# Kernel tuning notes

Measured on AMD Instinct MI355X. Metric: run time of the kernel, lower is better.

Reference implementation:

```python
import jax, jax.numpy as jnp
import numpy as np

N_NODES = 20000
N_EDGES = 320000
F_IN = 256      # num_features_mol
HIDDEN = 512    # hidden_size


def _glorot(key, shape):
    fan_in, fan_out = shape
    lim = jnp.sqrt(6.0 / (fan_in + fan_out)).astype(jnp.float32)
    return jax.random.uniform(key, shape, jnp.float32, -lim, lim)


def setup_inputs() -> dict:
    key = jax.random.key(0)
    ks = jax.random.split(key, 12)
    x = jax.random.normal(ks[0], (N_NODES, F_IN), jnp.float32)
    edge_index = jax.random.randint(ks[1], (2, N_EDGES), 0, N_NODES, dtype=jnp.int64)
    d1, d2, d3 = F_IN * 2, F_IN * 2, F_IN * 4  # 512, 512, 1024
    return {
        "x": x,
        "edge_index": edge_index,
        # SAGEConv layer i: lin_l (neighbor, with bias), lin_r (root, no bias)
        "Wl1": _glorot(ks[2], (F_IN, d1)), "bl1": jnp.zeros((d1,), jnp.float32),
        "Wr1": _glorot(ks[3], (F_IN, d1)),
        "Wl2": _glorot(ks[4], (d1, d2)), "bl2": jnp.zeros((d2,), jnp.float32),
        "Wr2": _glorot(ks[5], (d1, d2)),
        "Wl3": _glorot(ks[6], (d2, d3)), "bl3": jnp.zeros((d3,), jnp.float32),
        "Wr3": _glorot(ks[7], (d2, d3)),
        # mol_fc_g1: Linear(4*F -> hidden)
        "Wfc": _glorot(ks[8], (d3, HIDDEN)), "bfc": jnp.zeros((HIDDEN,), jnp.float32),
    }


def _sage_mean(x, src, dst, Wl, bl, Wr):
    # mean-aggregate neighbor features: messages flow src -> dst
    msg = x[src]                                               # [E, d]
    agg = jax.ops.segment_sum(msg, dst, num_segments=N_NODES)  # [N, d]
    cnt = jax.ops.segment_sum(jnp.ones((src.shape[0],), x.dtype), dst,
                              num_segments=N_NODES)            # [N]
    mean = agg / jnp.maximum(cnt, 1.0)[:, None]                # zero-deg -> 0
    return mean @ Wl + bl + x @ Wr


def reference(x, edge_index, Wl1, bl1, Wr1, Wl2, bl2, Wr2, Wl3, bl3, Wr3, Wfc, bfc):
    src, dst = edge_index[0], edge_index[1]
    h = jax.nn.relu(_sage_mean(x, src, dst, Wl1, bl1, Wr1))
    h = jax.nn.relu(_sage_mean(h, src, dst, Wl2, bl2, Wr2))
    h = jax.nn.relu(_sage_mean(h, src, dst, Wl3, bl3, Wr3))
    return h @ Wfc + bfc                                       # [N, HIDDEN]
```

## Files before the change

### kernel.cpp

```cpp
#include <hip/hip_runtime.h>
#include <hip/hip_bf16.h>


typedef __bf16 bf16x8 __attribute__((ext_vector_type(8)));
typedef float  f32x4  __attribute__((ext_vector_type(4)));

#define N_NODES 20000
#define N_EDGES 320000
#define MPAD 20096

__device__ __forceinline__ int clampi(int v, int lo, int hi) {
    return v < lo ? lo : (v > hi ? hi : v);
}

__device__ __forceinline__ void load16_lds(const void* g, void* l) {
    __builtin_amdgcn_global_load_lds(
        (const __attribute__((address_space(1))) void*)g,
        (__attribute__((address_space(3))) void*)l, 16, 0, 0);
}


__global__ void k_count(const int* __restrict__ ei, int E, int* __restrict__ cnt) {
    int e = blockIdx.x * blockDim.x + threadIdx.x;
    if (e < E) atomicAdd(&cnt[clampi(ei[E + e], 0, N_NODES - 1)], 1);
}

__global__ __launch_bounds__(1024) void k_scan_block(const int* __restrict__ cnt,
                                                     int* __restrict__ off,
                                                     int* __restrict__ bsum, int n) {
    __shared__ int sm[1024];
    int b = blockIdx.x, tid = threadIdx.x;
    int i = b * 1024 + tid;
    int v = (i < n) ? cnt[i] : 0;
    sm[tid] = v;
    __syncthreads();
    for (int s = 1; s < 1024; s <<= 1) {
        int t = (tid >= s) ? sm[tid - s] : 0;
        __syncthreads();
        sm[tid] += t;
        __syncthreads();
    }
    if (i < n) off[i] = sm[tid] - v;
    if (tid == 1023) bsum[b] = sm[1023];
}

__global__ void k_scan_carry(const int* __restrict__ bsum, int* __restrict__ carry,
                             int nb, int* __restrict__ off, int n) {
    if (threadIdx.x == 0 && blockIdx.x == 0) {
        int acc = 0;
        for (int b = 0; b < nb; ++b) { carry[b] = acc; acc += bsum[b]; }
        off[n] = acc;
    }
}

__global__ __launch_bounds__(1024) void k_scan_add(int* __restrict__ off,
                                                   int* __restrict__ cur,
                                                   const int* __restrict__ carry, int n) {
    int i = blockIdx.x * 1024 + threadIdx.x;
    if (i < n) {
        int v = off[i] + carry[blockIdx.x];
        off[i] = v;
        cur[i] = v;
    }
}

__global__ void k_fill(const int* __restrict__ ei, int E,
                       int* __restrict__ cur, int* __restrict__ csr) {
    int e = blockIdx.x * blockDim.x + threadIdx.x;
    if (e < E) {
        int dst = clampi(ei[E + e], 0, N_NODES - 1);
        int src = clampi(ei[e], 0, N_NODES - 1);
        int pos = atomicAdd(&cur[dst], 1);
        if (pos >= 0 && pos < E) csr[pos] = src;
    }
}


struct TDesc { const float* W; __bf16* Wt; int K, N, KT, koff, tile0; };
struct TDescs { TDesc d[7]; };

__global__ void k_transpose_all(TDescs ds) {
    __shared__ float tile[32][33];
    int b = blockIdx.x;
    int di = 0;
#pragma unroll
    for (int i = 1; i < 7; ++i)
        if (b >= ds.d[i].tile0) di = i;
    const float* W = ds.d[di].W;
    __bf16* Wt = ds.d[di].Wt;
    int N = ds.d[di].N, KT = ds.d[di].KT, koff = ds.d[di].koff;
    int t = b - ds.d[di].tile0;
    int ntn = N >> 5;
    int nb = (t % ntn) * 32, kb = (t / ntn) * 32;
    for (int i = 0; i < 32; i += 8) {
        int k = kb + threadIdx.y + i, n = nb + threadIdx.x;
        tile[threadIdx.y + i][threadIdx.x] = W[(size_t)k * N + n];
    }
    __syncthreads();
    for (int i = 0; i < 32; i += 8) {
        int n = nb + threadIdx.y + i, k = koff + kb + threadIdx.x;
        size_t o = (size_t)(n >> 7) * ((size_t)KT * 128) + (size_t)(k >> 3) * 1024 +
                   (size_t)((n & 127) * 8) + (k & 7);
        Wt[o] = (__bf16)tile[threadIdx.x][threadIdx.y + i];
    }
}


__global__ __launch_bounds__(256) void k_agg_f32(const float* __restrict__ xin,
                                                 const int* __restrict__ off,
                                                 const int* __restrict__ csr,
                                                 __bf16* __restrict__ acat) {
    __shared__ float sm[4][256];
    int node = blockIdx.x;
    int tid = threadIdx.x, slot = tid >> 6, lane = tid & 63;
    int c0 = lane * 4;
    int beg = off[node], end = off[node + 1];
    float a0 = 0.f, a1 = 0.f, a2 = 0.f, a3 = 0.f;
    for (int e = beg + slot; e < end; e += 4) {
        int s = csr[e];
        float4 v = *(const float4*)(xin + (size_t)s * 256 + c0);
        a0 += v.x; a1 += v.y; a2 += v.z; a3 += v.w;
    }
    sm[slot][c0] = a0; sm[slot][c0 + 1] = a1; sm[slot][c0 + 2] = a2; sm[slot][c0 + 3] = a3;
    __syncthreads();
    __bf16* base = acat + (size_t)(node >> 7) * (512 * 128) + (size_t)((node & 127) * 8);
    if (tid < 32) {
        float inv = 1.f / fmaxf((float)(end - beg), 1.f);
        int c = tid;
        __bf16 tmp[8];
#pragma unroll
        for (int i = 0; i < 8; ++i) {
            int col = c * 8 + i;
            tmp[i] = (__bf16)((sm[0][col] + sm[1][col] + sm[2][col] + sm[3][col]) * inv);
        }
        *(uint4*)(base + (size_t)c * 1024) = *(const uint4*)tmp;
    } else if (tid >= 64 && tid < 96) {
        int c = tid - 64;
        float4 u = *(const float4*)(xin + (size_t)node * 256 + c * 8);
        float4 w = *(const float4*)(xin + (size_t)node * 256 + c * 8 + 4);
        __bf16 tmp[8] = {(__bf16)u.x, (__bf16)u.y, (__bf16)u.z, (__bf16)u.w,
                         (__bf16)w.x, (__bf16)w.y, (__bf16)w.z, (__bf16)w.w};
        *(uint4*)(base + (size_t)(32 + c) * 1024) = *(const uint4*)tmp;
    }
}

__global__ __launch_bounds__(256) void k_agg_bf16(const __hip_bfloat16* __restrict__ hrm,
                                                  const int* __restrict__ off,
                                                  const int* __restrict__ csr,
                                                  __bf16* __restrict__ acat) {
    __shared__ float sm[4][512];
    int node = blockIdx.x;
    int tid = threadIdx.x, slot = tid >> 6, lane = tid & 63;
    int c0 = lane * 8;
    int beg = off[node], end = off[node + 1];
    float a[8] = {};
    for (int e = beg + slot; e < end; e += 4) {
        int s = csr[e];
        uint4 v = *(const uint4*)(hrm + (size_t)s * 512 + c0);
        const __hip_bfloat16* hb = (const __hip_bfloat16*)&v;
#pragma unroll
        for (int j = 0; j < 8; ++j) a[j] += __bfloat162float(hb[j]);
    }
#pragma unroll
    for (int j = 0; j < 8; ++j) sm[slot][c0 + j] = a[j];
    __syncthreads();
    if (tid < 64) {
        float inv = 1.f / fmaxf((float)(end - beg), 1.f);
        int c = tid;
        __bf16 tmp[8];
#pragma unroll
        for (int i = 0; i < 8; ++i) {
            int col = c * 8 + i;
            tmp[i] = (__bf16)((sm[0][col] + sm[1][col] + sm[2][col] + sm[3][col]) * inv);
        }
        *(uint4*)(acat + (size_t)(node >> 7) * (1024 * 128) +
                  (size_t)((node & 127) * 8) + (size_t)c * 1024) = *(const uint4*)tmp;
    }
}


template <bool RELU, int OUTMODE>
__global__ __launch_bounds__(256) void k_gemm(const __bf16* __restrict__ A, int K, int M,
                                              const __bf16* __restrict__ B,
                                              const float* __restrict__ bias,
                                              __bf16* __restrict__ osw, int Kc, int coff,
                                              __bf16* __restrict__ orm, int ldrm,
                                              float* __restrict__ of32, int ldf,
                                              int rtiles, int ctlog2) {
    constexpr int SMEM = (OUTMODE == 2) ? 34816 : 32768;
    __shared__ char smem[SMEM];
    __bf16* Alds = (__bf16*)smem;
    __bf16* Blds = (__bf16*)(smem + 16384);

    int bid = blockIdx.x;
    int xcd = bid & 7, local = bid >> 3;
    int cmask = (1 << ctlog2) - 1;
    int colTile = local & cmask;
    int rowTile = (local >> ctlog2) * 8 + xcd;
    if (rowTile >= rtiles) return;

    const __bf16* Atile = A + (size_t)rowTile * ((size_t)K * 128);
    const __bf16* Btile = B + (size_t)colTile * ((size_t)K * 128);

    int tid = threadIdx.x;
    int wave = tid >> 6, lane = tid & 63;
    int wr = wave >> 1, wc = wave & 1;
    int quad = lane >> 4, l16 = lane & 15;

    f32x4 acc[4][4] = {};

    for (int k0 = 0; k0 < K; k0 += 64) {
        __syncthreads();
        const __bf16* gA = Atile + (size_t)k0 * 128;
        const __bf16* gB = Btile + (size_t)k0 * 128;
#pragma unroll
        for (int j = 0; j < 4; ++j) {
            int slot = (j * 256 + tid) * 8;
            load16_lds(gA + slot, Alds + slot);
            load16_lds(gB + slot, Blds + slot);
        }
        __syncthreads();
#pragma unroll
        for (int sp = 0; sp < 2; ++sp) {
            bf16x8 af[4], bf[4];
#pragma unroll
            for (int mi = 0; mi < 4; ++mi)
                af[mi] = *(const bf16x8*)(Alds + sp * 4096 + quad * 1024 +
                                          (wr * 64 + mi * 16 + l16) * 8);
#pragma unroll
            for (int ni = 0; ni < 4; ++ni)
                bf[ni] = *(const bf16x8*)(Blds + sp * 4096 + quad * 1024 +
                                          (wc * 64 + ni * 16 + l16) * 8);
#pragma unroll
            for (int mi = 0; mi < 4; ++mi)
#pragma unroll
                for (int ni = 0; ni < 4; ++ni)
                    acc[mi][ni] = __builtin_amdgcn_mfma_f32_16x16x32_bf16(
                        af[mi], bf[ni], acc[mi][ni], 0, 0, 0);
        }
    }

    int col0 = colTile * 128;
    int row0 = rowTile * 128;
    __syncthreads();

    if (OUTMODE != 2) {
        __bf16* cb = (__bf16*)smem;
#pragma unroll
        for (int ni = 0; ni < 4; ++ni) {
            int ct = wc * 64 + ni * 16 + l16;
            float bv = bias[col0 + ct];
#pragma unroll
            for (int mi = 0; mi < 4; ++mi) {
                int rb = wr * 64 + mi * 16 + quad * 4;
#pragma unroll
                for (int r = 0; r < 4; ++r) {
                    float v = acc[mi][ni][r] + bv;
                    if (RELU) v = fmaxf(v, 0.f);
                    cb[(ct >> 3) * 1024 + (rb + r) * 8 + (ct & 7)] = (__bf16)v;
                }
            }
        }
        __syncthreads();
        __bf16* dst = osw + (size_t)rowTile * ((size_t)Kc * 128) +
                      (size_t)((coff + col0) >> 3) * 1024;
#pragma unroll
        for (int p2 = 0; p2 < 8; ++p2) {
            int idx = (p2 * 256 + tid) * 8;
            *(uint4*)(dst + idx) = *(const uint4*)(cb + idx);
        }
        if (OUTMODE == 1) {
#pragma unroll
            for (int p2 = 0; p2 < 8; ++p2) {
                int rr = p2 * 16 + (tid >> 4);
                int cc = tid & 15;
                *(uint4*)(orm + (size_t)(row0 + rr) * ldrm + col0 + cc * 8) =
                    *(const uint4*)(cb + cc * 1024 + rr * 8);
            }
        }
    } else {
        float* cf = (float*)smem;
#pragma unroll
        for (int h = 0; h < 2; ++h) {
            if (wc == h) {
#pragma unroll
                for (int ni = 0; ni < 4; ++ni) {
                    int ctl = ni * 16 + l16;
                    float bv = bias[col0 + h * 64 + ctl];
#pragma unroll
                    for (int mi = 0; mi < 4; ++mi) {
                        int rb = wr * 64 + mi * 16 + quad * 4;
#pragma unroll
                        for (int r = 0; r < 4; ++r) {
                            float v = acc[mi][ni][r] + bv;
                            if (RELU) v = fmaxf(v, 0.f);
                            cf[(rb + r) * 68 + ctl] = v;
                        }
                    }
                }
            }
            __syncthreads();
            int chunk = tid & 15, rl = tid >> 4;
#pragma unroll
            for (int p2 = 0; p2 < 8; ++p2) {
                int rt = p2 * 16 + rl;
                int row = row0 + rt;
                if (row < M) {
                    float4 v = *(const float4*)(cf + rt * 68 + chunk * 4);
                    *(float4*)(of32 + (size_t)row * ldf + col0 + h * 64 + chunk * 4) = v;
                }
            }
            __syncthreads();
        }
    }
}


extern "C" void kernel_launch(void* const* d_in, const int* in_sizes, int n_in,
                              void* d_out, int out_size, void* d_ws, size_t ws_size,
                              hipStream_t stream) {
    const float* x   = (const float*)d_in[0];
    const int*   ei  = (const int*)d_in[1];
    const float* Wl1 = (const float*)d_in[2];
    const float* bl1 = (const float*)d_in[3];
    const float* Wr1 = (const float*)d_in[4];
    const float* Wl2 = (const float*)d_in[5];
    const float* bl2 = (const float*)d_in[6];
    const float* Wr2 = (const float*)d_in[7];
    const float* Wl3 = (const float*)d_in[8];
    const float* bl3 = (const float*)d_in[9];
    const float* Wr3 = (const float*)d_in[10];
    const float* Wfc = (const float*)d_in[11];
    const float* bfc = (const float*)d_in[12];
    float* out = (float*)d_out;

    const int NN = N_NODES, E = N_EDGES;
    const int NB = (NN + 1023) / 1024;

    char* p = (char*)d_ws;
    auto alloc = [&](size_t bytes) {
        char* r = p;
        p += (bytes + 511) & ~(size_t)511;
        return r;
    };
    int* cnt   = (int*)alloc((size_t)NN * 4);
    int* off   = (int*)alloc((size_t)(NN + 1) * 4);
    int* cur   = (int*)alloc((size_t)NN * 4);
    int* csr   = (int*)alloc((size_t)E * 4);
    int* bsum  = (int*)alloc((size_t)NB * 4);
    int* carry = (int*)alloc((size_t)NB * 4);
    __bf16* Acat1 = (__bf16*)alloc((size_t)MPAD * 512 * 2);
    __bf16* Acat2 = (__bf16*)alloc((size_t)MPAD * 1024 * 2);
    __bf16* Acat3 = (__bf16*)alloc((size_t)MPAD * 1024 * 2);
    __bf16* Hrm   = (__bf16*)alloc((size_t)MPAD * 512 * 2);
    __bf16* Wt1 = (__bf16*)alloc((size_t)512 * 512 * 2);
    __bf16* Wt2 = (__bf16*)alloc((size_t)512 * 1024 * 2);
    __bf16* Wt3 = (__bf16*)alloc((size_t)1024 * 1024 * 2);
    __bf16* Wt4 = (__bf16*)alloc((size_t)512 * 1024 * 2);
    __bf16* H3 = Acat2;

    hipMemsetAsync(cnt, 0, (size_t)NN * 4, stream);
    k_count<<<(E + 255) / 256, 256, 0, stream>>>(ei, E, cnt);
    k_scan_block<<<NB, 1024, 0, stream>>>(cnt, off, bsum, NN);
    k_scan_carry<<<1, 64, 0, stream>>>(bsum, carry, NB, off, NN);
    k_scan_add<<<NB, 1024, 0, stream>>>(off, cur, carry, NN);
    k_fill<<<(E + 255) / 256, 256, 0, stream>>>(ei, E, cur, csr);

    TDescs td;
    td.d[0] = {Wl1, Wt1, 256, 512, 512, 0, 0};
    td.d[1] = {Wr1, Wt1, 256, 512, 512, 256, 128};
    td.d[2] = {Wl2, Wt2, 512, 512, 1024, 0, 256};
    td.d[3] = {Wr2, Wt2, 512, 512, 1024, 512, 512};
    td.d[4] = {Wl3, Wt3, 512, 1024, 1024, 0, 768};
    td.d[5] = {Wr3, Wt3, 512, 1024, 1024, 512, 1280};
    td.d[6] = {Wfc, Wt4, 1024, 512, 1024, 0, 1792};
    k_transpose_all<<<2304, dim3(32, 8), 0, stream>>>(td);

    int rtiles = (NN + 127) / 128;
    int rg = ((rtiles + 7) / 8) * 8;

    k_agg_f32<<<NN, 256, 0, stream>>>(x, off, csr, Acat1);
    k_gemm<true, 1><<<rg * 4, 256, 0, stream>>>(
        Acat1, 512, NN, Wt1, bl1, Acat2, 1024, 512, Hrm, 512, nullptr, 0, rtiles, 2);

    k_agg_bf16<<<NN, 256, 0, stream>>>((const __hip_bfloat16*)Hrm, off, csr, Acat2);
    k_gemm<true, 1><<<rg * 4, 256, 0, stream>>>(
        Acat2, 1024, NN, Wt2, bl2, Acat3, 1024, 512, Hrm, 512, nullptr, 0, rtiles, 2);

    k_agg_bf16<<<NN, 256, 0, stream>>>((const __hip_bfloat16*)Hrm, off, csr, Acat3);
    k_gemm<true, 0><<<rg * 8, 256, 0, stream>>>(
        Acat3, 1024, NN, Wt3, bl3, H3, 1024, 0, nullptr, 0, nullptr, 0, rtiles, 3);

    k_gemm<false, 2><<<rg * 4, 256, 0, stream>>>(
        H3, 1024, NN, Wt4, bfc, nullptr, 0, 0, nullptr, 0, out, 512, rtiles, 2);
}
```

Measured before the change: 446.4 us.

## Split aggregation into column slices with one wave per node

The neighbor-mean aggregation kernels are restructured so that each block handles 4 nodes (one per wave) and one of 8 column slices, and the two halves of each wave split the edge list. The shared-memory reduction and block barrier are replaced by a single cross-half shuffle. The aim is more parallelism and no LDS sync per node. The cost is narrower per-thread loads (scalar f32, or 4-byte bf16 pairs instead of 16-byte vectors), each edge index being re-read by 8 blocks, and scalar scattered stores into the swizzled output.

```diff
diff --git a/kernel.cpp b/kernel.cpp
--- a/kernel.cpp
+++ b/kernel.cpp
@@ -106,75 +106,59 @@
 }
 
 
-__global__ __launch_bounds__(256) void k_agg_f32(const float* __restrict__ xin,
-                                                 const int* __restrict__ off,
-                                                 const int* __restrict__ csr,
-                                                 __bf16* __restrict__ acat) {
-    __shared__ float sm[4][256];
-    int node = blockIdx.x;
-    int tid = threadIdx.x, slot = tid >> 6, lane = tid & 63;
-    int c0 = lane * 4;
+__global__ __launch_bounds__(256) void k_agg1(const float* __restrict__ x,
+                                              const int* __restrict__ off,
+                                              const int* __restrict__ csr,
+                                              __bf16* __restrict__ acat) {
+    int bid = blockIdx.x;
+    int slice = bid & 7, group = bid >> 3;
+    int wave = threadIdx.x >> 6, lane = threadIdx.x & 63;
+    int node = group * 4 + wave;
+    int half = lane >> 5, l = lane & 31;
     int beg = off[node], end = off[node + 1];
-    float a0 = 0.f, a1 = 0.f, a2 = 0.f, a3 = 0.f;
-    for (int e = beg + slot; e < end; e += 4) {
-        int s = csr[e];
-        float4 v = *(const float4*)(xin + (size_t)s * 256 + c0);
-        a0 += v.x; a1 += v.y; a2 += v.z; a3 += v.w;
-    }
-    sm[slot][c0] = a0; sm[slot][c0 + 1] = a1; sm[slot][c0 + 2] = a2; sm[slot][c0 + 3] = a3;
-    __syncthreads();
-    __bf16* base = acat + (size_t)(node >> 7) * (512 * 128) + (size_t)((node & 127) * 8);
-    if (tid < 32) {
+    const float* xs = x + slice * 32 + l;
+    float acc = 0.f;
+    for (int e = beg + half; e < end; e += 2)
+        acc += xs[(size_t)csr[e] * 256];
+    acc += __shfl_xor(acc, 32, 64);
+    if (half == 0) {
         float inv = 1.f / fmaxf((float)(end - beg), 1.f);
-        int c = tid;
-        __bf16 tmp[8];
-#pragma unroll
-        for (int i = 0; i < 8; ++i) {
-            int col = c * 8 + i;
-            tmp[i] = (__bf16)((sm[0][col] + sm[1][col] + sm[2][col] + sm[3][col]) * inv);
-        }
-        *(uint4*)(base + (size_t)c * 1024) = *(const uint4*)tmp;
-    } else if (tid >= 64 && tid < 96) {
-        int c = tid - 64;
-        float4 u = *(const float4*)(xin + (size_t)node * 256 + c * 8);
-        float4 w = *(const float4*)(xin + (size_t)node * 256 + c * 8 + 4);
-        __bf16 tmp[8] = {(__bf16)u.x, (__bf16)u.y, (__bf16)u.z, (__bf16)u.w,
-                         (__bf16)w.x, (__bf16)w.y, (__bf16)w.z, (__bf16)w.w};
-        *(uint4*)(base + (size_t)(32 + c) * 1024) = *(const uint4*)tmp;
-    }
-}
-
-__global__ __launch_bounds__(256) void k_agg_bf16(const __hip_bfloat16* __restrict__ hrm,
-                                                  const int* __restrict__ off,
-                                                  const int* __restrict__ csr,
-                                                  __bf16* __restrict__ acat) {
-    __shared__ float sm[4][512];
-    int node = blockIdx.x;
-    int tid = threadIdx.x, slot = tid >> 6, lane = tid & 63;
-    int c0 = lane * 8;
+        size_t base = (size_t)(node >> 7) * (512 * 128) + (size_t)((node & 127) * 8);
+        int k = slice * 32 + l;
+        acat[base + (size_t)(k >> 3) * 1024 + (k & 7)] = (__bf16)(acc * inv);
+        int k2 = 256 + k;
+        float xv = x[(size_t)node * 256 + slice * 32 + l];
+        acat[base + (size_t)(k2 >> 3) * 1024 + (k2 & 7)] = (__bf16)xv;
+    }
+}
+
+__global__ __launch_bounds__(256) void k_agg2(const __bf16* __restrict__ hrm,
+                                              const int* __restrict__ off,
+                                              const int* __restrict__ csr,
+                                              __bf16* __restrict__ acat) {
+    int bid = blockIdx.x;
+    int slice = bid & 7, group = bid >> 3;
+    int wave = threadIdx.x >> 6, lane = threadIdx.x & 63;
+    int node = group * 4 + wave;
+    int half = lane >> 5, l = lane & 31;
     int beg = off[node], end = off[node + 1];
-    float a[8] = {};
-    for (int e = beg + slot; e < end; e += 4) {
-        int s = csr[e];
-        uint4 v = *(const uint4*)(hrm + (size_t)s * 512 + c0);
-        const __hip_bfloat16* hb = (const __hip_bfloat16*)&v;
-#pragma unroll
-        for (int j = 0; j < 8; ++j) a[j] += __bfloat162float(hb[j]);
-    }
-#pragma unroll
-    for (int j = 0; j < 8; ++j) sm[slot][c0 + j] = a[j];
-    __syncthreads();
-    if (tid < 64) {
+    const __bf16* hs = hrm + slice * 64 + l * 2;
+    float a0 = 0.f, a1 = 0.f;
+    for (int e = beg + half; e < end; e += 2) {
+        unsigned int v = *(const unsigned int*)(hs + (size_t)csr[e] * 512);
+        union { unsigned int u; __hip_bfloat162 b; } cv; cv.u = v;
+        a0 += __bfloat162float(cv.b.x);
+        a1 += __bfloat162float(cv.b.y);
+    }
+    a0 += __shfl_xor(a0, 32, 64);
+    a1 += __shfl_xor(a1, 32, 64);
+    if (half == 0) {
         float inv = 1.f / fmaxf((float)(end - beg), 1.f);
-        int c = tid;
-        __bf16 tmp[8];
-#pragma unroll
-        for (int i = 0; i < 8; ++i) {
-            int col = c * 8 + i;
-            tmp[i] = (__bf16)((sm[0][col] + sm[1][col] + sm[2][col] + sm[3][col]) * inv);
-        }
-        *(uint4*)(acat + (size_t)(node >> 7) * (1024 * 128) +
-                  (size_t)((node & 127) * 8) + (size_t)c * 1024) = *(const uint4*)tmp;
+        int k = slice * 64 + l * 2;
+        __bf16* dst = acat + (size_t)(node >> 7) * (1024 * 128) +
+                      (size_t)((node & 127) * 8) + (size_t)(k >> 3) * 1024 + (k & 7);
+        dst[0] = (__bf16)(a0 * inv);
+        dst[1] = (__bf16)(a1 * inv);
     }
 }
 
@@ -378,16 +362,17 @@
 
     int rtiles = (NN + 127) / 128;
     int rg = ((rtiles + 7) / 8) * 8;
-
-    k_agg_f32<<<NN, 256, 0, stream>>>(x, off, csr, Acat1);
+    int aggGrid = (NN / 4) * 8;
+
+    k_agg1<<<aggGrid, 256, 0, stream>>>(x, off, csr, Acat1);
     k_gemm<true, 1><<<rg * 4, 256, 0, stream>>>(
         Acat1, 512, NN, Wt1, bl1, Acat2, 1024, 512, Hrm, 512, nullptr, 0, rtiles, 2);
 
-    k_agg_bf16<<<NN, 256, 0, stream>>>((const __hip_bfloat16*)Hrm, off, csr, Acat2);
+    k_agg2<<<aggGrid, 256, 0, stream>>>(Hrm, off, csr, Acat2);
     k_gemm<true, 1><<<rg * 4, 256, 0, stream>>>(
         Acat2, 1024, NN, Wt2, bl2, Acat3, 1024, 512, Hrm, 512, nullptr, 0, rtiles, 2);
 
-    k_agg_bf16<<<NN, 256, 0, stream>>>((const __hip_bfloat16*)Hrm, off, csr, Acat3);
+    k_agg2<<<aggGrid, 256, 0, stream>>>(Hrm, off, csr, Acat3);
     k_gemm<true, 0><<<rg * 8, 256, 0, stream>>>(
         Acat3, 1024, NN, Wt3, bl3, H3, 1024, 0, nullptr, 0, nullptr, 0, rtiles, 3);
 
```

New measurement: 538.4 us. 1.21x slower.
